# Kernel optimization log

Hardware: AMD Instinct MI355X
Metric: run time of the kernel (lower is better)

The kernel has to match this reference:

```python
import jax, jax.numpy as jnp
import numpy as np

NUM_ON_STATES = 65536
LATENT_DIM = 512


def setup_inputs() -> dict:
    key = jax.random.key(0)
    k1, k2, k3, k4 = jax.random.split(key, 4)
    input_mu = jax.random.normal(k1, (LATENT_DIM,), dtype=jnp.float32)
    input_sig = jax.random.uniform(k2, (LATENT_DIM,), dtype=jnp.float32)
    on_mus = jax.random.normal(k3, (NUM_ON_STATES, LATENT_DIM), dtype=jnp.float32)
    on_sigs = jax.random.uniform(k4, (NUM_ON_STATES, LATENT_DIM), dtype=jnp.float32)
    on_states = jnp.stack([on_mus, on_sigs], axis=-1)  # [N, D, 2]
    return {"input_mu": input_mu, "input_sig": input_sig, "on_states": on_states}


def reference(input_mu, input_sig, on_states):
    # on_states: [N, D, 2] -> codebook means / sigmas
    mus = on_states[..., 0]   # [N, D]
    sigs = on_states[..., 1]  # [N, D]
    # squared 2-Wasserstein distance between diagonal Gaussians, per codebook entry
    # (vectorized form of the original per-entry python loop)
    dists = jnp.sum((input_mu - mus) ** 2 + (input_sig - sigs) ** 2, axis=1)  # [N]
    # mode == 'softmin': softmin(d) = softmax(-d)
    ps = jax.nn.softmax(-dists)                     # [N]
    quantised = ps @ mus                            # [D], softmin-weighted codebook mean
    # commitment / reference losses (straight-through style detach pattern)
    loss_enc = jnp.mean((jax.lax.stop_gradient(quantised) - input_mu) ** 2)
    loss_ref = jnp.mean((quantised - jax.lax.stop_gradient(input_mu)) ** 2)
    return (quantised, loss_enc, loss_ref, dists)
```

## Files before the change

### kernel.cpp

```cpp
#include <hip/hip_runtime.h>
#include <float.h>

#define NSTATES 65536
#define DIM 512
#define K1_BLOCKS 512
#define K1_THREADS 256
#define WPB 4
#define ROWS_PER_BLOCK (NSTATES / K1_BLOCKS)
#define ROWS_PER_WAVE (ROWS_PER_BLOCK / WPB)
#define K2_THREADS 512

__global__ __launch_bounds__(K1_THREADS) void k_dist(
    const float* __restrict__ imu, const float* __restrict__ isig,
    const float* __restrict__ st, float* __restrict__ dists,
    float* __restrict__ ws_q, float* __restrict__ ws_m, float* __restrict__ ws_s)
{
    const int lane = threadIdx.x & 63;
    const int wid  = threadIdx.x >> 6;

    float im[8], isg[8];
    #pragma unroll
    for (int k = 0; k < 4; ++k) {
        const int d0 = 128 * k + 2 * lane;
        im[2*k]    = imu[d0];   im[2*k+1]  = imu[d0 + 1];
        isg[2*k]   = isig[d0];  isg[2*k+1] = isig[d0 + 1];
    }

    float m = FLT_MAX, s = 0.f;
    float q[8] = {0.f, 0.f, 0.f, 0.f, 0.f, 0.f, 0.f, 0.f};

    const int row0 = blockIdx.x * ROWS_PER_BLOCK + wid * ROWS_PER_WAVE;
    for (int r = 0; r < ROWS_PER_WAVE; ++r) {
        const int n = row0 + r;
        const float4* p = reinterpret_cast<const float4*>(st + (size_t)n * (2 * DIM));
        const float4 v0 = p[lane];
        const float4 v1 = p[64  + lane];
        const float4 v2 = p[128 + lane];
        const float4 v3 = p[192 + lane];

        float d = 0.f, a, b;
        a = v0.x - im[0]; b = v0.y - isg[0]; d += a*a + b*b;
        a = v0.z - im[1]; b = v0.w - isg[1]; d += a*a + b*b;
        a = v1.x - im[2]; b = v1.y - isg[2]; d += a*a + b*b;
        a = v1.z - im[3]; b = v1.w - isg[3]; d += a*a + b*b;
        a = v2.x - im[4]; b = v2.y - isg[4]; d += a*a + b*b;
        a = v2.z - im[5]; b = v2.w - isg[5]; d += a*a + b*b;
        a = v3.x - im[6]; b = v3.y - isg[6]; d += a*a + b*b;
        a = v3.z - im[7]; b = v3.w - isg[7]; d += a*a + b*b;

        #pragma unroll
        for (int off = 32; off >= 1; off >>= 1) d += __shfl_xor(d, off, 64);

        if (lane == 0) dists[n] = d;

        const float mn   = fminf(m, d);
        const float cold = __expf(mn - m);
        const float w    = __expf(mn - d);
        s = s * cold + w;
        q[0] = q[0] * cold + w * v0.x;  q[1] = q[1] * cold + w * v0.z;
        q[2] = q[2] * cold + w * v1.x;  q[3] = q[3] * cold + w * v1.z;
        q[4] = q[4] * cold + w * v2.x;  q[5] = q[5] * cold + w * v2.z;
        q[6] = q[6] * cold + w * v3.x;  q[7] = q[7] * cold + w * v3.z;
        m = mn;
    }

    __shared__ float lq[WPB][DIM];
    __shared__ float lm[WPB], ls[WPB];
    #pragma unroll
    for (int k = 0; k < 4; ++k) {
        const int d0 = 128 * k + 2 * lane;
        lq[wid][d0]     = q[2*k];
        lq[wid][d0 + 1] = q[2*k + 1];
    }
    if (lane == 0) { lm[wid] = m; ls[wid] = s; }
    __syncthreads();

    const int t = threadIdx.x;
    const float M = fminf(fminf(lm[0], lm[1]), fminf(lm[2], lm[3]));
    float qa = 0.f, qb = 0.f;
    #pragma unroll
    for (int w2 = 0; w2 < WPB; ++w2) {
        const float f = __expf(M - lm[w2]);
        qa += lq[w2][t]       * f;
        qb += lq[w2][t + 256] * f;
    }
    ws_q[blockIdx.x * DIM + t]       = qa;
    ws_q[blockIdx.x * DIM + t + 256] = qb;
    if (t == 0) {
        float stot = 0.f;
        #pragma unroll
        for (int w2 = 0; w2 < WPB; ++w2) stot += ls[w2] * __expf(M - lm[w2]);
        ws_m[blockIdx.x] = M;
        ws_s[blockIdx.x] = stot;
    }
}

__global__ __launch_bounds__(K2_THREADS) void k_final(
    const float* __restrict__ imu,
    const float* __restrict__ ws_q, const float* __restrict__ ws_m,
    const float* __restrict__ ws_s, float* __restrict__ out)
{
    __shared__ float f_sh[K1_BLOCKS];
    __shared__ float red[8];
    __shared__ float Msh, Ssh;
    const int t = threadIdx.x;
    const int lane = t & 63, wid = t >> 6;

    float mv = ws_m[t];
    #pragma unroll
    for (int off = 32; off >= 1; off >>= 1) mv = fminf(mv, __shfl_xor(mv, off, 64));
    if (lane == 0) red[wid] = mv;
    __syncthreads();
    if (t == 0) {
        float x = red[0];
        #pragma unroll
        for (int i = 1; i < 8; ++i) x = fminf(x, red[i]);
        Msh = x;
    }
    __syncthreads();
    const float M = Msh;

    const float f = __expf(M - ws_m[t]);
    f_sh[t] = f;
    float sp = ws_s[t] * f;
    #pragma unroll
    for (int off = 32; off >= 1; off >>= 1) sp += __shfl_xor(sp, off, 64);
    __syncthreads();
    if (lane == 0) red[wid] = sp;
    __syncthreads();
    if (t == 0) {
        float x = 0.f;
        #pragma unroll
        for (int i = 0; i < 8; ++i) x += red[i];
        Ssh = x;
    }
    __syncthreads();
    const float S = Ssh;

    float qa = 0.f;
    #pragma unroll 8
    for (int b = 0; b < K1_BLOCKS; ++b) qa += ws_q[b * DIM + t] * f_sh[b];

    const float quant = qa / S;
    out[t] = quant;

    const float diff = quant - imu[t];
    float e = diff * diff;
    #pragma unroll
    for (int off = 32; off >= 1; off >>= 1) e += __shfl_xor(e, off, 64);
    __syncthreads();
    if (lane == 0) red[wid] = e;
    __syncthreads();
    if (t == 0) {
        float x = 0.f;
        #pragma unroll
        for (int i = 0; i < 8; ++i) x += red[i];
        x *= (1.0f / DIM);
        out[DIM]     = x;
        out[DIM + 1] = x;
    }
}

extern "C" void kernel_launch(void* const* d_in, const int* in_sizes, int n_in,
                              void* d_out, int out_size, void* d_ws, size_t ws_size,
                              hipStream_t stream) {
    const float* imu  = (const float*)d_in[0];
    const float* isig = (const float*)d_in[1];
    const float* st   = (const float*)d_in[2];
    float* out = (float*)d_out;
    float* ws  = (float*)d_ws;

    float* ws_q = ws;
    float* ws_m = ws_q + K1_BLOCKS * DIM;
    float* ws_s = ws_m + K1_BLOCKS;

    k_dist<<<K1_BLOCKS, K1_THREADS, 0, stream>>>(imu, isig, st,
                                                 out + DIM + 2, ws_q, ws_m, ws_s);
    k_final<<<1, K2_THREADS, 0, stream>>>(imu, ws_q, ws_m, ws_s, out);
}
```

Before: 390.9 us.

## Double-buffer row loads with nontemporal loads and process two rows per iteration

Raises the distance kernel to 512 threads (8 waves per block) and software-pipelines the row stream, prefetching the next two rows into registers while the current pair is reduced. Loads use nontemporal hints to avoid polluting the cache with the streamed 256 MB codebook, and two rows share one online-softmax rescale. The block-level merge is generalized to 8 waves. Register pressure goes up from holding 16 float4s, and occupancy is bounded by the launch_bounds hint.

After: 368.8 us. 1.06x faster.

```diff
diff --git a/kernel.cpp b/kernel.cpp
--- a/kernel.cpp
+++ b/kernel.cpp
@@ -4,13 +4,16 @@
 #define NSTATES 65536
 #define DIM 512
 #define K1_BLOCKS 512
-#define K1_THREADS 256
-#define WPB 4
+#define K1_THREADS 512
+#define WPB 8
 #define ROWS_PER_BLOCK (NSTATES / K1_BLOCKS)
 #define ROWS_PER_WAVE (ROWS_PER_BLOCK / WPB)
 #define K2_THREADS 512
 
-__global__ __launch_bounds__(K1_THREADS) void k_dist(
+typedef float f4 __attribute__((ext_vector_type(4)));
+#define NTL(addr) __builtin_nontemporal_load(addr)
+
+__global__ __launch_bounds__(K1_THREADS, 4) void k_dist(
     const float* __restrict__ imu, const float* __restrict__ isig,
     const float* __restrict__ st, float* __restrict__ dists,
     float* __restrict__ ws_q, float* __restrict__ ws_m, float* __restrict__ ws_s)
@@ -30,38 +33,60 @@
     float q[8] = {0.f, 0.f, 0.f, 0.f, 0.f, 0.f, 0.f, 0.f};
 
     const int row0 = blockIdx.x * ROWS_PER_BLOCK + wid * ROWS_PER_WAVE;
-    for (int r = 0; r < ROWS_PER_WAVE; ++r) {
+    const f4* p = reinterpret_cast<const f4*>(st + (size_t)row0 * (2 * DIM)) + lane;
+
+    f4 cur[8], nxt[8];
+    #pragma unroll
+    for (int k = 0; k < 4; ++k) {
+        cur[k]     = NTL(p + 64 * k);
+        cur[4 + k] = NTL(p + 256 + 64 * k);
+    }
+
+    #pragma unroll 1
+    for (int r = 0; r < ROWS_PER_WAVE; r += 2) {
+        const int rn = (r + 2 < ROWS_PER_WAVE) ? (r + 2) : r;
+        const f4* pn = p + (size_t)rn * 256;
+        #pragma unroll
+        for (int k = 0; k < 4; ++k) {
+            nxt[k]     = NTL(pn + 64 * k);
+            nxt[4 + k] = NTL(pn + 256 + 64 * k);
+        }
+
+        float d0 = 0.f, d1 = 0.f;
+        #pragma unroll
+        for (int k = 0; k < 4; ++k) {
+            float x, y;
+            x = cur[k].x - im[2*k];       y = cur[k].y - isg[2*k];       d0 += x*x + y*y;
+            x = cur[k].z - im[2*k+1];     y = cur[k].w - isg[2*k+1];     d0 += x*x + y*y;
+            x = cur[4+k].x - im[2*k];     y = cur[4+k].y - isg[2*k];     d1 += x*x + y*y;
+            x = cur[4+k].z - im[2*k+1];   y = cur[4+k].w - isg[2*k+1];   d1 += x*x + y*y;
+        }
+        #pragma unroll
+        for (int off = 32; off >= 1; off >>= 1) {
+            d0 += __shfl_xor(d0, off, 64);
+            d1 += __shfl_xor(d1, off, 64);
+        }
+
         const int n = row0 + r;
-        const float4* p = reinterpret_cast<const float4*>(st + (size_t)n * (2 * DIM));
-        const float4 v0 = p[lane];
-        const float4 v1 = p[64  + lane];
-        const float4 v2 = p[128 + lane];
-        const float4 v3 = p[192 + lane];
-
-        float d = 0.f, a, b;
-        a = v0.x - im[0]; b = v0.y - isg[0]; d += a*a + b*b;
-        a = v0.z - im[1]; b = v0.w - isg[1]; d += a*a + b*b;
-        a = v1.x - im[2]; b = v1.y - isg[2]; d += a*a + b*b;
-        a = v1.z - im[3]; b = v1.w - isg[3]; d += a*a + b*b;
-        a = v2.x - im[4]; b = v2.y - isg[4]; d += a*a + b*b;
-        a = v2.z - im[5]; b = v2.w - isg[5]; d += a*a + b*b;
-        a = v3.x - im[6]; b = v3.y - isg[6]; d += a*a + b*b;
-        a = v3.z - im[7]; b = v3.w - isg[7]; d += a*a + b*b;
-
-        #pragma unroll
-        for (int off = 32; off >= 1; off >>= 1) d += __shfl_xor(d, off, 64);
-
-        if (lane == 0) dists[n] = d;
-
-        const float mn   = fminf(m, d);
+        if (lane == 0) {
+            dists[n]     = d0;
+            dists[n + 1] = d1;
+        }
+
+        const float mn   = fminf(m, fminf(d0, d1));
         const float cold = __expf(mn - m);
-        const float w    = __expf(mn - d);
-        s = s * cold + w;
-        q[0] = q[0] * cold + w * v0.x;  q[1] = q[1] * cold + w * v0.z;
-        q[2] = q[2] * cold + w * v1.x;  q[3] = q[3] * cold + w * v1.z;
-        q[4] = q[4] * cold + w * v2.x;  q[5] = q[5] * cold + w * v2.z;
-        q[6] = q[6] * cold + w * v3.x;  q[7] = q[7] * cold + w * v3.z;
+        const float w0   = __expf(mn - d0);
+        const float w1   = __expf(mn - d1);
+        s = s * cold + w0 + w1;
+        #pragma unroll
+        for (int k = 0; k < 4; ++k) {
+            q[2*k]   = q[2*k]   * cold + w0 * cur[k].x + w1 * cur[4+k].x;
+            q[2*k+1] = q[2*k+1] * cold + w0 * cur[k].z + w1 * cur[4+k].z;
+        }
         m = mn;
+
+        #pragma unroll
+        for (int k = 0; k < 8; ++k) cur[k] = nxt[k];
     }
 
     __shared__ float lq[WPB][DIM];
@@ -76,16 +101,13 @@
     __syncthreads();
 
     const int t = threadIdx.x;
-    const float M = fminf(fminf(lm[0], lm[1]), fminf(lm[2], lm[3]));
-    float qa = 0.f, qb = 0.f;
-    #pragma unroll
-    for (int w2 = 0; w2 < WPB; ++w2) {
-        const float f = __expf(M - lm[w2]);
-        qa += lq[w2][t]       * f;
-        qb += lq[w2][t + 256] * f;
-    }
-    ws_q[blockIdx.x * DIM + t]       = qa;
-    ws_q[blockIdx.x * DIM + t + 256] = qb;
+    float M = lm[0];
+    #pragma unroll
+    for (int w2 = 1; w2 < WPB; ++w2) M = fminf(M, lm[w2]);
+    float qa = 0.f;
+    #pragma unroll
+    for (int w2 = 0; w2 < WPB; ++w2) qa += lq[w2][t] * __expf(M - lm[w2]);
+    ws_q[blockIdx.x * DIM + t] = qa;
     if (t == 0) {
         float stot = 0.f;
         #pragma unroll
```
